# Performance work log

Measured on AMD Instinct MI355X. Metric: run time of the kernel, lower is better.

Reference implementation:

```python
import jax, jax.numpy as jnp
import numpy as np

NLAYERS, NHEADS, NFEAT, HDIM = 2, 8, 512, 64
ALPHA = 0.2
NEG = -9e15


def setup_inputs() -> dict:
    key = jax.random.key(0)
    ks = jax.random.split(key, 20)
    B, Ng, Nc, Nq = 4, 1024, 1024, 256
    s = 0.05
    inp = {
        "gloss": jax.random.normal(ks[0], (B, Ng, NFEAT), jnp.float32),
        "clip": jax.random.normal(ks[1], (B, Nc, NFEAT), jnp.float32),
        "question": jax.random.normal(ks[2], (B, Nq, NFEAT), jnp.float32),
        "gloss2clipadj": jax.random.randint(ks[3], (B, Ng, Nc), 0, 2, jnp.int32),
        "gloss2questionadj": jax.random.randint(ks[4], (B, Ng, Nq), 0, 2, jnp.int32),
    }
    # per-layer, per-head attention params: W [L,H,F,D], a split halves a1/a2 [L,H,D]
    for i, name in enumerate(["c2g", "g2q", "q2g"]):
        inp[name + "_W"] = jax.random.normal(ks[5 + i], (NLAYERS, NHEADS, NFEAT, HDIM), jnp.float32) * s
        inp[name + "_a1"] = jax.random.normal(ks[8 + i], (NLAYERS, NHEADS, HDIM), jnp.float32) * s
        inp[name + "_a2"] = jax.random.normal(ks[11 + i], (NLAYERS, NHEADS, HDIM), jnp.float32) * s
    # 4 FusionLayers per encoder layer (G2C, C2G, G2Q, Q2G), each with W,U,Wf,Uf [F,F]
    for i, name in enumerate(["fus_W", "fus_U", "fus_Wf", "fus_Uf"]):
        inp[name] = jax.random.normal(ks[14 + i], (NLAYERS, 4, NFEAT, NFEAT), jnp.float32) * s
    return inp


def _attn(q, kv, adj, W, a1, a2):
    # multi-head GAT-style additive cross attention; W [H,F,D], q [B,N,F], kv [B,M,F], adj [B,N,M]
    Wq = jnp.einsum('bnf,hfd->bhnd', q, W)
    Wk = jnp.einsum('bmf,hfd->bhmd', kv, W)
    e = jax.nn.leaky_relu(
        jnp.einsum('bhnd,hd->bhn', Wq, a1)[:, :, :, None]
        + jnp.einsum('bhmd,hd->bhm', Wk, a2)[:, :, None, :], ALPHA)
    e = jnp.where(adj[:, None, :, :] > 0, e, NEG)
    att = jax.nn.softmax(e, axis=2)  # torch F.softmax(dim=1) on [B,N,M]: query axis (faithful)
    h = jax.nn.elu(jnp.einsum('bhnm,bhmd->bhnd', att, Wk))
    B, H, N, D = h.shape
    return jnp.transpose(h, (0, 2, 1, 3)).reshape(B, N, H * D)  # concat heads


def _fusion(a, b, W, U, Wf, Uf):
    new_a = a @ W + b @ U
    f = jax.nn.sigmoid(a @ Wf + b @ Uf)
    return f * new_a + (1.0 - f) * a  # dropout is identity at inference


def reference(gloss, clip, question, gloss2clipadj, gloss2questionadj,
              c2g_W, c2g_a1, c2g_a2, g2q_W, g2q_a1, g2q_a2, q2g_W, q2g_a1, q2g_a2,
              fus_W, fus_U, fus_Wf, fus_Uf):
    g2c_f = gloss2clipadj.astype(gloss.dtype)
    g2q_T = jnp.transpose(gloss2questionadj, (0, 2, 1))
    for l in range(NLAYERS):
        gloss_same = jnp.einsum('bnm,bnf->bmf', g2c_f, gloss)  # adj^T @ gloss
        clip_1 = _fusion(clip, gloss_same, fus_W[l, 0], fus_U[l, 0], fus_Wf[l, 0], fus_Uf[l, 0])
        clip_agg = _attn(gloss, clip, gloss2clipadj, c2g_W[l], c2g_a1[l], c2g_a2[l])
        gloss_1 = _fusion(gloss, clip_agg, fus_W[l, 1], fus_U[l, 1], fus_Wf[l, 1], fus_Uf[l, 1])
        gloss_agg = _attn(question, gloss, g2q_T, g2q_W[l], g2q_a1[l], g2q_a2[l])
        question_1 = _fusion(question, gloss_agg, fus_W[l, 2], fus_U[l, 2], fus_Wf[l, 2], fus_Uf[l, 2])
        question_agg = _attn(gloss, question, gloss2questionadj, q2g_W[l], q2g_a1[l], q2g_a2[l])
        gloss_2 = _fusion(gloss_1, question_agg, fus_W[l, 3], fus_U[l, 3], fus_Wf[l, 3], fus_Uf[l, 3])
        gloss, clip, question = gloss_2, clip_1, question_1
    return gloss, clip, question
```

## Files before the change

### kernel.cpp

```cpp
#include <hip/hip_runtime.h>
#include <math.h>

#define NFEAT 512
#define NHEADS 8
#define HDIM 64
#define NB 4
#define NG 1024
#define NC 1024
#define NQ 256
#define NEGV -9e15f
#define CHUNKS 16
#define FF ((size_t)NFEAT*NFEAT)
#define LSTR 36
#define SEG 2304

typedef _Float16 v8h __attribute__((ext_vector_type(8)));
typedef float v4f __attribute__((ext_vector_type(4)));
#define MFMA16(a,b,c) __builtin_amdgcn_mfma_f32_16x16x32_f16((a),(b),(c),0,0,0)

#define GLDS(g, l) __builtin_amdgcn_global_load_lds( \
    (__attribute__((address_space(1))) void*)(g), \
    (__attribute__((address_space(3))) void*)(l), 16, 0, 0)

__device__ __forceinline__ int ldsw(int row, int quad){
    return row*32 + (((quad) ^ ((row>>1)&3)) << 3);
}

__device__ __forceinline__ float lrelu(float x){ return fmaxf(x, 0.2f*x); }
__device__ __forceinline__ unsigned short f2h(float x){ union{_Float16 h; unsigned short u;} v; v.h = (_Float16)x; return v.u; }
__device__ __forceinline__ float h2f(unsigned short u){ union{_Float16 h; unsigned short u;} v; v.u = u; return (float)v.h; }

__global__ __launch_bounds__(256) void cvt_h_k(const float* __restrict__ src, unsigned short* __restrict__ dst){
    int idx = blockIdx.x*256 + threadIdx.x;
    const float4* s = (const float4*)(src + (size_t)idx*8);
    float4 a = s[0], b = s[1];
    ushort4 p0{f2h(a.x),f2h(a.y),f2h(a.z),f2h(a.w)};
    ushort4 p1{f2h(b.x),f2h(b.y),f2h(b.z),f2h(b.w)};
    *(ushort4*)(dst + (size_t)idx*8) = p0;
    *(ushort4*)(dst + (size_t)idx*8 + 4) = p1;
}

__global__ __launch_bounds__(256) void cvt_hl_k(const float* __restrict__ src,
    unsigned short* __restrict__ dstHi, unsigned short* __restrict__ dstLo){
    int idx = blockIdx.x*256 + threadIdx.x;
// ... 64 lines not shown
        int idx = (r & 15)*256 + tid;
        int h = idx >> 9;
        const float* Wp = W + (size_t)idx*64;
        float s1 = 0.f, s2 = 0.f;
        #pragma unroll
        for (int d = 0; d < 64; ++d){ float w = Wp[d]; s1 += w*a1[(h<<6)+d]; s2 += w*a2[(h<<6)+d]; }
        wa13[a*4096 + idx] = s1; wa23[a*4096 + idx] = s2;
        return;
    }
    int a = bx >> 6, bxl = bx & 63;
    const float* W = (a==0?W0:a==1?W1:W2);
    unsigned short* WT = WT3 + (size_t)a*FF;
    int h = bxl >> 3, f0 = (bxl & 7)*64;
    __shared__ float sT[64][65];
    #pragma unroll
    for (int it = 0; it < 4; ++it){
        int idx = it*256 + tid;
        int r = idx >> 4, c4 = idx & 15;
        float4 v = *(const float4*)(W + ((size_t)h*512 + f0 + r)*64 + c4*4);
        sT[r][c4*4+0]=v.x; sT[r][c4*4+1]=v.y; sT[r][c4*4+2]=v.z; sT[r][c4*4+3]=v.w;
    }
    __syncthreads();
    #pragma unroll
    for (int it = 0; it < 2; ++it){
        int idx = it*256 + tid;
        int dd = idx >> 3, c8 = idx & 7;
        ushort4 p0{f2h(sT[c8*8+0][dd]),f2h(sT[c8*8+1][dd]),f2h(sT[c8*8+2][dd]),f2h(sT[c8*8+3][dd])};
        ushort4 p1{f2h(sT[c8*8+4][dd]),f2h(sT[c8*8+5][dd]),f2h(sT[c8*8+6][dd]),f2h(sT[c8*8+7][dd])};
        unsigned short* o = WT + ((size_t)h*64 + dd)*512 + f0 + c8*8;
        *(ushort4*)o = p0; *(ushort4*)(o+4) = p1;
    }
}

__global__ __launch_bounds__(256) void adjT_h_k(const int* __restrict__ adj, unsigned short* __restrict__ dst){
    int b = blockIdx.z;
    int c0 = blockIdx.x*64, g0 = blockIdx.y*64;
    __shared__ int sI[64][65];
    int tid = threadIdx.x;
    #pragma unroll
    for (int it = 0; it < 4; ++it){
        int idx = it*256 + tid;
        int r = idx >> 4, c4 = idx & 15;
        int4 v = *(const int4*)(adj + ((size_t)b*NG + g0 + r)*NC + c0 + c4*4);
        sI[r][c4*4+0]=v.x; sI[r][c4*4+1]=v.y; sI[r][c4*4+2]=v.z; sI[r][c4*4+3]=v.w;
    }
    __syncthreads();
    #pragma unroll
    for (int it = 0; it < 2; ++it){
        int idx = it*256 + tid;
        int dd = idx >> 3, c8 = idx & 7;
        ushort4 p0, p1;
        #pragma unroll
        for (int j = 0; j < 4; ++j) (&p0.x)[j] = sI[c8*8+j][dd] > 0 ? (unsigned short)0x3C00 : (unsigned short)0;
        #pragma unroll
        for (int j = 0; j < 4; ++j) (&p1.x)[j] = sI[c8*8+4+j][dd] > 0 ? (unsigned short)0x3C00 : (unsigned short)0;
        unsigned short* o = dst + ((size_t)b*NC + c0 + dd)*NG + g0 + c8*8;
        *(ushort4*)o = p0; *(ushort4*)(o+4) = p1;
    }
}

__global__ __launch_bounds__(256) void adjT_int_k(const int* __restrict__ adj, int* __restrict__ dst){
    int b = blockIdx.z;
    int q0 = blockIdx.x*64, g0 = blockIdx.y*64;
    __shared__ int sI[64][65];
    int tid = threadIdx.x;
    #pragma unroll
    for (int it = 0; it < 4; ++it){
        int idx = it*256 + tid;
        int r = idx >> 4, c4 = idx & 15;
        int4 v = *(const int4*)(adj + ((size_t)b*NG + g0 + r)*NQ + q0 + c4*4);
        sI[r][c4*4+0]=v.x; sI[r][c4*4+1]=v.y; sI[r][c4*4+2]=v.z; sI[r][c4*4+3]=v.w;
    }
    __syncthreads();
    #pragma unroll
    for (int it = 0; it < 4; ++it){
        int idx = it*256 + tid;
        int dd = idx >> 4, c4 = idx & 15;
        int4 v{sI[c4*4+0][dd], sI[c4*4+1][dd], sI[c4*4+2][dd], sI[c4*4+3][dd]};
        *(int4*)(dst + ((size_t)b*NQ + q0 + dd)*NG + g0 + c4*4) = v;
    }
}

__global__ __launch_bounds__(256) void bm_int_k(const int* __restrict__ adj, unsigned long long* __restrict__ out){
    int w = threadIdx.x >> 6, lane = threadIdx.x & 63;
    #pragma unroll
    for (int i = 0; i < 4; ++i){
        size_t seg = (size_t)blockIdx.x*16 + i*4 + w;
        int v = adj[seg*64 + lane];
        unsigned long long m = __ballot(v > 0);
        if (lane == 0) out[seg] = m;
    }
}

__global__ __launch_bounds__(256) void bm_h_k(const unsigned short* __restrict__ adj, unsigned long long* __restrict__ out){
    int w = threadIdx.x >> 6, lane = threadIdx.x & 63;
    #pragma unroll
    for (int i = 0; i < 4; ++i){
        size_t seg = (size_t)blockIdx.x*16 + i*4 + w;
        unsigned short v = adj[seg*64 + lane];
        unsigned long long m = __ballot(v != 0);
        if (lane == 0) out[seg] = m;
    }
}

__global__ __launch_bounds__(256) void actT_hl_k(const float* __restrict__ src,
    unsigned short* __restrict__ dstHi, unsigned short* __restrict__ dstLo, int Nrows){
    int b = blockIdx.z;
    int f0 = blockIdx.x*64, g0 = blockIdx.y*64;
    __shared__ float sF[64][65];
    int tid = threadIdx.x;
    #pragma unroll
    for (int it = 0; it < 4; ++it){
        int idx = it*256 + tid;
        int r = idx >> 4, c4 = idx & 15;
        float4 v = *(const float4*)(src + ((size_t)b*Nrows + g0 + r)*512 + f0 + c4*4);
        sF[r][c4*4+0]=v.x; sF[r][c4*4+1]=v.y; sF[r][c4*4+2]=v.z; sF[r][c4*4+3]=v.w;
    }
    __syncthreads();
    #pragma unroll
    for (int it = 0; it < 2; ++it){
        int idx = it*256 + tid;
        int dd = idx >> 3, c8 = idx & 7;
        unsigned short hi[8], lo[8];
        #pragma unroll
        for (int j = 0; j < 8; ++j){
            float x = sF[c8*8+j][dd];
            hi[j] = f2h(x);
            lo[j] = f2h(x - h2f(hi[j]));
        }
        size_t oo = ((size_t)b*512 + f0 + dd)*Nrows + g0 + c8*8;
        *(ushort4*)(dstHi+oo)   = ushort4{hi[0],hi[1],hi[2],hi[3]};
        *(ushort4*)(dstHi+oo+4) = ushort4{hi[4],hi[5],hi[6],hi[7]};
        *(ushort4*)(dstLo+oo)   = ushort4{lo[0],lo[1],lo[2],lo[3]};
        *(ushort4*)(dstLo+oo+4) = ushort4{lo[4],lo[5],lo[6],lo[7]};
    }
}

__global__ __launch_bounds__(256) void scores3_k(
    const unsigned short* __restrict__ g, const unsigned short* __restrict__ c,
    const unsigned short* __restrict__ q,
    const float* __restrict__ wa13, const float* __restrict__ wa23,
    float* __restrict__ qs3, float* __restrict__ ks3){
    int lane = threadIdx.x & 63;
    int grow = blockIdx.x*4 + (threadIdx.x >> 6);
    int b = grow / 4608; int r = grow - b*4608;
    const unsigned short* X; const float* wa; float* out; int n, oOff, rowsX;
    if (r < SEG){
        out = qs3;
        if (r < 1024)      { X=g; wa=wa13;        n=r;        oOff=0;    rowsX=NG; }
        else if (r < 1280) { X=q; wa=wa13+4096;   n=r-1024;   oOff=1024; rowsX=NQ; }
        else               { X=g; wa=wa13+8192;   n=r-1280;   oOff=1280; rowsX=NG; }
    } else {
        out = ks3; r -= SEG;
        if (r < 1024)      { X=c; wa=wa23;        n=r;        oOff=0;    rowsX=NC; }
        else if (r < 2048) { X=g; wa=wa23+4096;   n=r-1024;   oOff=1024; rowsX=NG; }
        else               { X=q; wa=wa23+8192;   n=r-2048;   oOff=2048; rowsX=NQ; }
    }
    const unsigned short* Xr = X + ((size_t)b*rowsX + n)*NFEAT;
    float p[NHEADS];
    #pragma unroll
    for (int h = 0; h < NHEADS; ++h) p[h] = 0.f;
    #pragma unroll
    for (int cc = 0; cc < 8; ++cc){
        float x = h2f(Xr[(cc<<6) + lane]);
        #pragma unroll
        for (int h = 0; h < NHEADS; ++h) p[h] += x * wa[(h<<9) + (cc<<6) + lane];
    }
// ... 28 lines not shown
    size_t aRow = (size_t)(r0 + sr)*512 + sq*8;
    size_t bRow = (size_t)(c0 + sr)*512 + sq*8;
    v4f acc[4];
    #pragma unroll
    for (int cf = 0; cf < 4; ++cf) acc[cf] = (v4f)0.f;
    GLDS(aG + aRow, &aS[0][w << 9]);
    GLDS(bG + bRow, &bS[0][w << 9]);
    __syncthreads();
    int buf = 0;
    for (int s = 0; s < 16; ++s){
        if (s < 15){
            int ktn = (s + 1) << 5;
            GLDS(aG + aRow + ktn, &aS[buf^1][w << 9]);
            GLDS(bG + bRow + ktn, &bS[buf^1][w << 9]);
        }
        v8h af = *(const v8h*)&aS[buf][ldsw(w*16 + lrow, quad)];
        #pragma unroll
        for (int cf = 0; cf < 4; ++cf){
            v8h bf = *(const v8h*)&bS[buf][ldsw(cf*16 + lrow, quad)];
            acc[cf] = MFMA16(af, bf, acc[cf]);
        }
        __syncthreads();
        buf ^= 1;
    }
    #pragma unroll
    for (int cf = 0; cf < 4; ++cf){
        int colg = c0 + cf*16 + lrow;
        int rbase = r0 + w*16 + quad*4;
        ushort4 pk{f2h(acc[cf][0]), f2h(acc[cf][1]), f2h(acc[cf][2]), f2h(acc[cf][3])};
        *(ushort4*)&WkT3[((size_t)b*512 + colg)*SEG + mOff + rbase] = pk;
    }
}

__global__ __launch_bounds__(256) void colstat3_k(
    const unsigned* __restrict__ bm_cg, const unsigned* __restrict__ bm_gq,
    const unsigned* __restrict__ bm_qg,
    const float* __restrict__ qs3, const float* __restrict__ ks3,
    float* __restrict__ pcm, float* __restrict__ psum){
    int x = blockIdx.x, b = blockIdx.z;
    const unsigned* bm; int Mrows, N, N32, mOff, qOff;
    if (x < 256)      { bm=bm_cg; Mrows=NC; N=NG; N32=NG/32; mOff=0;    qOff=0; }
    else if (x < 512) { x-=256; bm=bm_gq; Mrows=NG; N=NQ; N32=NQ/32; mOff=1024; qOff=1024; }
    else              { x-=512; bm=bm_qg; Mrows=NQ; N=NG; N32=NG/32; mOff=2048; qOff=1280; }
    int mt = x >> 4, ch = x & 15;
    int chunk = N / CHUNKS, subl = chunk >> 2;
    int ml = threadIdx.x & 63; int m = mt*64 + ml;
    int g = threadIdx.x >> 6;
    int n0 = ch*chunk + g*subl;
    __shared__ float sQ[64][8];
    for (int t2 = threadIdx.x; t2 < chunk*8; t2 += 256)
        sQ[t2>>3][t2&7] = qs3[((size_t)b*SEG + qOff + ch*chunk)*8 + t2];
    float ksv[8];
    size_t mo = ((size_t)b*SEG + mOff + m)*8;
    #pragma unroll
    for (int h = 0; h < 8; ++h) ksv[h] = ks3[mo+h];
    unsigned word = bm[((size_t)b*Mrows + m)*N32 + (n0>>5)];
    unsigned bits = (word >> (n0 & 31)) & ((1u << subl) - 1u);
    __syncthreads();
    int nb = g*subl;
    float mx[8];
    #pragma unroll
    for (int h = 0; h < 8; ++h) mx[h] = -INFINITY;
    for (int i = 0; i < subl; ++i){
        if ((bits >> i) & 1){
            #pragma unroll
            for (int h = 0; h < 8; ++h) mx[h] = fmaxf(mx[h], sQ[nb+i][h]);
        }
    }
    float cm[8], s[8];
    #pragma unroll
    for (int h = 0; h < 8; ++h){
        cm[h] = bits ? lrelu(mx[h] + ksv[h]) : NEGV;
        s[h] = 0.f;
    }
    for (int i = 0; i < subl; ++i){
        bool on = (bits >> i) & 1;
        #pragma unroll
        for (int h = 0; h < 8; ++h){
            float e = on ? lrelu(sQ[nb+i][h] + ksv[h]) : NEGV;
            s[h] += __expf(e - cm[h]);
        }
    }
    __shared__ float scm[4][64][8], ssm[4][64][8];
    #pragma unroll
    for (int h = 0; h < 8; ++h){ scm[g][ml][h] = cm[h]; ssm[g][ml][h] = s[h]; }
    __syncthreads();
    if (g == 0){
        #pragma unroll
        for (int h = 0; h < 8; ++h){
            float c0 = scm[0][ml][h], c1 = scm[1][ml][h], c2 = scm[2][ml][h], c3 = scm[3][ml][h];
            float CM = fmaxf(fmaxf(c0, c1), fmaxf(c2, c3));
            float S = ssm[0][ml][h]*__expf(c0-CM) + ssm[1][ml][h]*__expf(c1-CM)
                    + ssm[2][ml][h]*__expf(c2-CM) + ssm[3][ml][h]*__expf(c3-CM);
            size_t o = (((size_t)b*CHUNKS + ch)*SEG + mOff + m)*8 + h;
            pcm[o] = CM; psum[o] = S;
        }
    }
}

__global__ __launch_bounds__(256) void colfin3_k(const float* __restrict__ pcm, const float* __restrict__ psum,
    const float* __restrict__ ks3, float* __restrict__ ksh, float* __restrict__ cmh,
    float* __restrict__ ish){
    int idx = blockIdx.x*256 + threadIdx.x;
    const int m8 = SEG*8;
    int b = idx / m8, rem = idx - b*m8;
    int m = rem >> 3, h = rem & 7;
    size_t base = (size_t)b*CHUNKS*m8 + rem;
    float c[CHUNKS], s[CHUNKS];
    #pragma unroll
    for (int ch = 0; ch < CHUNKS; ++ch){
        c[ch] = pcm[base + (size_t)ch*m8];
        s[ch] = psum[base + (size_t)ch*m8];
    }
    float CM = c[0];
    #pragma unroll
    for (int ch = 1; ch < CHUNKS; ++ch) CM = fmaxf(CM, c[ch]);
    float S = 0.f;
    #pragma unroll
    for (int ch = 0; ch < CHUNKS; ++ch) S += s[ch]*__expf(c[ch] - CM);
    size_t o = ((size_t)b*8 + h)*SEG + m;
    ksh[o] = ks3[idx]; cmh[o] = CM; ish[o] = 1.f/S;
}

template<int MULTI>
__global__ __launch_bounds__(256) void fusion_all_k(
    const unsigned short* __restrict__ aHi, const unsigned short* __restrict__ aLo,
    const unsigned short* __restrict__ bHi, const unsigned short* __restrict__ bLo,
    const unsigned short* __restrict__ Whi, const unsigned short* __restrict__ Wlo,
    unsigned short* __restrict__ dst, unsigned short* __restrict__ dstLo,
    unsigned short* __restrict__ dstT, unsigned short* __restrict__ dstTLo,
    float* __restrict__ dstF, int rows){
    int nY = rows >> 6;
    int ppg = (nY * NB) >> 3;
    int F = blockIdx.x;
    int xcd = F & 7, t = F >> 3;
    int c0i = t / ppg;
    int p = xcd + ((t - c0i*ppg) << 3);
    int r0 = (p % nY) << 6, c0 = c0i << 6;
    int b = p / nY;
    int tid = threadIdx.x;
    __shared__ alignas(16) unsigned short aHs[2048], bHs[2048];
    __shared__ alignas(16) unsigned short aLs[MULTI ? 2048 : 16], bLs[MULTI ? 2048 : 16];
    __shared__ alignas(16) unsigned short wHs[8192];
    __shared__ alignas(16) unsigned short wLs[MULTI ? 8192 : 16];
    size_t actOff = (size_t)b*rows*512;
    const unsigned short* aHG = aHi + actOff;
    const unsigned short* bHG = bHi + actOff;
    const unsigned short* aLG = aLo ? aLo + actOff : nullptr;
    const unsigned short* bLG = bLo ? bLo + actOff : nullptr;
    bool hasALo = MULTI && (aLG != nullptr);
    bool hasBLo = MULTI && (bLG != nullptr);
    int w = tid >> 6, lane = tid & 63;
    int wr = w >> 1, wc = w & 1;
    int lrow = lane & 15, quad = lane >> 4;
    int sr = tid >> 2;
    int sq = (tid & 3) ^ ((sr >> 1) & 3);
    size_t aRow = (size_t)(r0 + sr)*512 + sq*8;
    size_t wPk = (size_t)c0i*16*8192 + (size_t)sr*32 + sq*8;
    unsigned short* ldsA  = &aHs[w << 9];
    unsigned short* ldsB  = &bHs[w << 9];
    unsigned short* ldsAL = &aLs[MULTI ? (w << 9) : 0];
    unsigned short* ldsBL = &bLs[MULTI ? (w << 9) : 0];
    v4f accN[2][2], accF[2][2];
    #pragma unroll
    for (int r = 0; r < 2; ++r)
        #pragma unroll
        for (int cf = 0; cf < 2; ++cf){ accN[r][cf] = (v4f)0.f; accF[r][cf] = (v4f)0.f; }
    for (int kt = 0; kt < 512; kt += 32){
        __syncthreads();
        GLDS(aHG + aRow + kt, ldsA);
        GLDS(bHG + aRow + kt, ldsB);
        if (hasALo) GLDS(aLG + aRow + kt, ldsAL);
        if (hasBLo) GLDS(bLG + aRow + kt, ldsBL);
        size_t wk = wPk + (size_t)(kt >> 5)*8192;
        #pragma unroll
        for (int m = 0; m < 4; ++m){
            GLDS(Whi + wk + (m<<11), &wHs[(m<<11) + (w<<9)]);
            if (MULTI) GLDS(Wlo + wk + (m<<11), &wLs[MULTI ? ((m<<11) + (w<<9)) : 0]);
        }
        __syncthreads();
        v8h ah[2], bh[2], al[2], bl[2];
        #pragma unroll
        for (int r = 0; r < 2; ++r){
            int ao = ldsw(wr*32 + r*16 + lrow, quad);
            ah[r] = *(const v8h*)&aHs[ao];
            bh[r] = *(const v8h*)&bHs[ao];
            if (hasALo) al[r] = *(const v8h*)&aLs[ao];
            if (hasBLo) bl[r] = *(const v8h*)&bLs[ao];
        }
        #pragma unroll
        for (int cf = 0; cf < 2; ++cf){
            int wo = ldsw(wc*32 + cf*16 + lrow, quad);
            v8h w0 = *(const v8h*)&wHs[wo];
            v8h w1 = *(const v8h*)&wHs[2048 + wo];
            v8h w2 = *(const v8h*)&wHs[4096 + wo];
            v8h w3 = *(const v8h*)&wHs[6144 + wo];
            v8h l0, l1, l2, l3;
            if (MULTI){
                l0 = *(const v8h*)&wLs[wo];
                l1 = *(const v8h*)&wLs[2048 + wo];
                l2 = *(const v8h*)&wLs[4096 + wo];
                l3 = *(const v8h*)&wLs[6144 + wo];
            }
            #pragma unroll
            for (int r = 0; r < 2; ++r){
                accN[r][cf] = MFMA16(ah[r], w0, accN[r][cf]);
                accN[r][cf] = MFMA16(bh[r], w1, accN[r][cf]);
                accF[r][cf] = MFMA16(ah[r], w2, accF[r][cf]);
                accF[r][cf] = MFMA16(bh[r], w3, accF[r][cf]);
                if (MULTI){
                    if (hasALo){ accN[r][cf] = MFMA16(al[r], w0, accN[r][cf]); accF[r][cf] = MFMA16(al[r], w2, accF[r][cf]); }
                    if (hasBLo){ accN[r][cf] = MFMA16(bl[r], w1, accN[r][cf]); accF[r][cf] = MFMA16(bl[r], w3, accF[r][cf]); }
                    accN[r][cf] = MFMA16(ah[r], l0, accN[r][cf]);
                    accN[r][cf] = MFMA16(bh[r], l1, accN[r][cf]);
                    accF[r][cf] = MFMA16(ah[r], l2, accF[r][cf]);
                    accF[r][cf] = MFMA16(bh[r], l3, accF[r][cf]);
                }
            }
        }
    }
    #pragma unroll
    for (int r = 0; r < 2; ++r)
        #pragma unroll
        for (int cf = 0; cf < 2; ++cf){
            int colg = c0 + wc*32 + cf*16 + lrow;
            int rbase = r0 + wr*32 + r*16 + quad*4;
            float o4[4];
            #pragma unroll
            for (int reg = 0; reg < 4; ++reg){
                float f = 1.f/(1.f + __expf(-accF[r][cf][reg]));
                size_t ai = (size_t)(rbase+reg)*512 + colg;
                float ao = h2f(aHG[ai]);
                if (aLG) ao += h2f(aLG[ai]);
                o4[reg] = f*accN[r][cf][reg] + (1.f - f)*ao;
                size_t oo = ((size_t)b*rows + rbase + reg)*512 + colg;
                unsigned short hv = f2h(o4[reg]);
                dst[oo] = hv;
                if (dstLo) dstLo[oo] = f2h(o4[reg] - h2f(hv));
                if (dstF) dstF[oo] = o4[reg];
            }
            if (dstT){
                unsigned short h0 = f2h(o4[0]), h1 = f2h(o4[1]), h2 = f2h(o4[2]), h3 = f2h(o4[3]);
                size_t to = ((size_t)b*512 + colg)*rows + rbase;
                *(ushort4*)&dstT[to] = ushort4{h0,h1,h2,h3};
                if (dstTLo)
                    *(ushort4*)&dstTLo[to] = ushort4{f2h(o4[0]-h2f(h0)), f2h(o4[1]-h2f(h1)),
                                                     f2h(o4[2]-h2f(h2)), f2h(o4[3]-h2f(h3))};
            }
        }
}

__global__ __launch_bounds__(256) void gemmT_mfma_k(
    const unsigned short* __restrict__ A, size_t aStride,
    const unsigned short* __restrict__ BT, const unsigned short* __restrict__ BT2, size_t bStride,
    int K, int rowsPB,
    unsigned short* __restrict__ outRM, unsigned short* __restrict__ outLo,
    unsigned short* __restrict__ outT){
    int b = blockIdx.z;
    int r0 = blockIdx.y*64, c0 = blockIdx.x*64;
    int tid = threadIdx.x;
    __shared__ alignas(16) unsigned short aS[2][2048], bS[2][2048];
    const unsigned short* aG = A + (size_t)b*aStride;
    const unsigned short* bG0 = BT + (size_t)b*bStride;
    const unsigned short* bG1 = BT2 ? BT2 + (size_t)b*bStride : nullptr;
    int w = tid >> 6, lane = tid & 63;
    int lrow = lane & 15, quad = lane >> 4;
    int sr = tid >> 2;
    int sq = (tid & 3) ^ ((sr >> 1) & 3);
    size_t aRow = (size_t)(r0 + sr)*K + sq*8;
    size_t bRow = (size_t)(c0 + sr)*K + sq*8;
    int spp = K >> 5;
    int nsteps = (BT2 ? 2 : 1)*spp;
    v4f acc[4];
    #pragma unroll
    for (int cf = 0; cf < 4; ++cf) acc[cf] = (v4f)0.f;
    GLDS(aG + aRow, &aS[0][w << 9]);
    GLDS(bG0 + bRow, &bS[0][w << 9]);
    __syncthreads();
    int buf = 0;
    for (int s = 0; s < nsteps; ++s){
// ... 162 lines not shown
    const float* in_gloss = (const float*)d_in[0];
    const float* in_clip  = (const float*)d_in[1];
    const float* in_q     = (const float*)d_in[2];
    const int*   adj_gc   = (const int*)d_in[3];
    const int*   adj_gq   = (const int*)d_in[4];
    const float* c2gW  = (const float*)d_in[5];
    const float* c2ga1 = (const float*)d_in[6];
    const float* c2ga2 = (const float*)d_in[7];
    const float* g2qW  = (const float*)d_in[8];
    const float* g2qa1 = (const float*)d_in[9];
    const float* g2qa2 = (const float*)d_in[10];
    const float* q2gW  = (const float*)d_in[11];
    const float* q2ga1 = (const float*)d_in[12];
    const float* q2ga2 = (const float*)d_in[13];
    const float* fusW  = (const float*)d_in[14];
    const float* fusU  = (const float*)d_in[15];
    const float* fusWf = (const float*)d_in[16];
    const float* fusUf = (const float*)d_in[17];
    float* out = (float*)d_out;
    float* out_gloss = out;
    float* out_clip  = out + (size_t)NB*NG*NFEAT;
    float* out_q     = out + (size_t)NB*NG*NFEAT*2;

    char* wsB = (char*)d_ws;
    size_t off = 0;
    auto alloc = [&](size_t bytes){ void* p = wsB + off; off += (bytes + 255) & ~(size_t)255; return p; };
    float* wa13  = (float*)alloc(3*4096*4);
    float* wa23  = (float*)alloc(3*4096*4);
    float* qs3   = (float*)alloc((size_t)NB*SEG*8*4);
    float* ks3   = (float*)alloc((size_t)NB*SEG*8*4);
    float* ksh3  = (float*)alloc((size_t)NB*8*SEG*4);
    float* cmh3  = (float*)alloc((size_t)NB*8*SEG*4);
    float* ish3  = (float*)alloc((size_t)NB*8*SEG*4);
    float* pcm   = (float*)alloc((size_t)NB*CHUNKS*SEG*8*4);
    float* psum  = (float*)alloc((size_t)NB*CHUNKS*SEG*8*4);
    unsigned short* WflatT3 = (unsigned short*)alloc((size_t)3*FF*2);
    unsigned short* WkT3    = (unsigned short*)alloc((size_t)NB*512*SEG*2);
    unsigned short* wtAll   = (unsigned short*)alloc((size_t)32*FF*2);
    unsigned short* wtAllLo = (unsigned short*)alloc((size_t)32*FF*2);
    unsigned short* adjTgc  = (unsigned short*)alloc((size_t)NB*NC*NG*2);
    unsigned short* g_bf0   = (unsigned short*)alloc((size_t)NB*NG*NFEAT*2);
    unsigned short* gLo0    = (unsigned short*)alloc((size_t)NB*NG*NFEAT*2);
    unsigned short* g_bf1   = (unsigned short*)alloc((size_t)NB*NG*NFEAT*2);
    unsigned short* gLo1    = (unsigned short*)alloc((size_t)NB*NG*NFEAT*2);
    unsigned short* gT      = (unsigned short*)alloc((size_t)NB*NFEAT*NG*2);
    unsigned short* gTlo    = (unsigned short*)alloc((size_t)NB*NFEAT*NG*2);
    unsigned short* gA_bf   = (unsigned short*)alloc((size_t)NB*NG*NFEAT*2);
    unsigned short* gALo    = (unsigned short*)alloc((size_t)NB*NG*NFEAT*2);
    unsigned short* c_bf0   = (unsigned short*)alloc((size_t)NB*NC*NFEAT*2);
    unsigned short* cLo0    = (unsigned short*)alloc((size_t)NB*NC*NFEAT*2);
    unsigned short* c_bf1   = (unsigned short*)alloc((size_t)NB*NC*NFEAT*2);
    unsigned short* cLo1    = (unsigned short*)alloc((size_t)NB*NC*NFEAT*2);
    unsigned short* q_bf0   = (unsigned short*)alloc((size_t)NB*NQ*NFEAT*2);
    unsigned short* q_bf1   = (unsigned short*)alloc((size_t)NB*NQ*NFEAT*2);
    unsigned short* agg_bf  = (unsigned short*)alloc((size_t)NB*NG*NFEAT*2);
    unsigned short* aggLo   = (unsigned short*)alloc((size_t)NB*NG*NFEAT*2);
    int* adjTgq = (int*)alloc((size_t)NB*NQ*NG*4);
    unsigned* bm_gc = (unsigned*)alloc((size_t)NB*NG*(NC/32)*4);
    unsigned* bm_cg = (unsigned*)alloc((size_t)NB*NC*(NG/32)*4);
    unsigned* bm_gq = (unsigned*)alloc((size_t)NB*NG*(NQ/32)*4);
    unsigned* bm_qg = (unsigned*)alloc((size_t)NB*NQ*(NG/32)*4);
    (void)ws_size; (void)in_sizes; (void)n_in; (void)out_size;

    const size_t HFD = (size_t)NHEADS*NFEAT*HDIM;
    const size_t HD  = (size_t)NHEADS*HDIM;

    wtT_k<<<2048, 256, 0, stream>>>(fusW, fusU, fusWf, fusUf, wtAll, wtAllLo);
    adjT_h_k<<<dim3(NC/64, NG/64, NB), 256, 0, stream>>>(adj_gc, adjTgc);
    adjT_int_k<<<dim3(NQ/64, NG/64, NB), 256, 0, stream>>>(adj_gq, adjTgq);
    bm_int_k<<<(NB*NG*NC/64)/16, 256, 0, stream>>>(adj_gc, (unsigned long long*)bm_gc);
    bm_int_k<<<(NB*NG*NQ/64)/16, 256, 0, stream>>>(adj_gq, (unsigned long long*)bm_gq);
    bm_int_k<<<(NB*NQ*NG/64)/16, 256, 0, stream>>>(adjTgq, (unsigned long long*)bm_qg);
    bm_h_k<<<(NB*NC*NG/64)/16, 256, 0, stream>>>(adjTgc, (unsigned long long*)bm_cg);
    cvt_hl_k<<<(NB*NG*NFEAT)/2048, 256, 0, stream>>>(in_gloss, g_bf0, gLo0);
    cvt_hl_k<<<(NB*NC*NFEAT)/2048, 256, 0, stream>>>(in_clip,  c_bf0, cLo0);
    cvt_h_k<<<(NB*NQ*NFEAT)/2048, 256, 0, stream>>>(in_q,     q_bf0);
    actT_hl_k<<<dim3(8, NG/64, NB), 256, 0, stream>>>(in_gloss, gT, gTlo, NG);

    auto run_fusion = [&](const unsigned short* a, const unsigned short* aLo,
                          const unsigned short* bb, const unsigned short* bLo, int rows,
                          int l, int i, int npass,
                          unsigned short* dst, unsigned short* dstLo,
                          unsigned short* dstT, unsigned short* dstTLo, float* dstF){
        const unsigned short* Whi = wtAll   + (size_t)((l*4 + i)*4)*FF;
        const unsigned short* Wlo = wtAllLo + (size_t)((l*4 + i)*4)*FF;
        if (npass == 3)
            fusion_all_k<1><<<dim3(8*(rows/64)*NB), 256, 0, stream>>>(
                a, aLo, bb, bLo, Whi, Wlo, dst, dstLo, dstT, dstTLo, dstF, rows);
        else
            fusion_all_k<0><<<dim3(8*(rows/64)*NB), 256, 0, stream>>>(
                a, aLo, bb, bLo, Whi, Wlo, dst, dstLo, dstT, dstTLo, dstF, rows);
    };

    for (int l = 0; l < 2; ++l){
        const unsigned short* g_cur = (l == 0) ? g_bf0 : g_bf1;
        const unsigned short* gLoC  = (l == 0) ? gLo0  : gLo1;
        const unsigned short* c_cur = (l == 0) ? c_bf0 : c_bf1;
        const unsigned short* cLoC  = (l == 0) ? cLo0  : cLo1;
        const unsigned short* q_cur = (l == 0) ? q_bf0 : q_bf1;
        unsigned short* g_nxt = (l == 0) ? g_bf1 : g_bf0;
        unsigned short* gLoN  = (l == 0) ? gLo1  : nullptr;
        unsigned short* c_nxt = (l == 0) ? c_bf1 : c_bf0;
        unsigned short* cLoN  = (l == 0) ? cLo1  : nullptr;
        unsigned short* q_nxt = (l == 0) ? q_bf1 : q_bf0;
        float* gF = (l == 1) ? out_gloss : nullptr;
        float* cF = (l == 1) ? out_clip  : nullptr;
        float* qF = (l == 1) ? out_q     : nullptr;

        prep_attnW3_k<<<240, 256, 0, stream>>>(
            c2gW + l*HFD, c2ga1 + l*HD, c2ga2 + l*HD,
            g2qW + l*HFD, g2qa1 + l*HD, g2qa2 + l*HD,
            q2gW + l*HFD, q2ga1 + l*HD, q2ga2 + l*HD,
            WflatT3, wa13, wa23);
        scores3_k<<<(NB*4608)/4, 256, 0, stream>>>(g_cur, c_cur, q_cur, wa13, wa23, qs3, ks3);
        wkt3_mfma_k<<<dim3(8, 36, NB), 256, 0, stream>>>(c_cur, g_cur, q_cur, WflatT3, WkT3);
        colstat3_k<<<dim3(576, 1, NB), 256, 0, stream>>>(bm_cg, bm_gq, bm_qg, qs3, ks3, pcm, psum);
        colfin3_k<<<(NB*SEG*8)/256, 256, 0, stream>>>(pcm, psum, ks3, ksh3, cmh3, ish3);

        gemmT_mfma_k<<<dim3(8, NC/64, NB), 256, 0, stream>>>(adjTgc, (size_t)NC*NG, gT, gTlo,
                                                             (size_t)512*NG, NG, NC,
                                                             agg_bf, aggLo, nullptr);
        run_fusion(c_cur, cLoC, agg_bf, aggLo, NC, l, 0, 3,
                   c_nxt, cLoN, nullptr, nullptr, cF);
        attn_mfma_k<<<(NG/64)*32, 256, 0, stream>>>(bm_gc, NC/32, qs3, 0, ksh3, cmh3, ish3, 0,
                                                    WkT3, agg_bf, NG, NC);
        run_fusion(g_cur, gLoC, agg_bf, nullptr, NG, l, 1, 1,
                   gA_bf, gALo, nullptr, nullptr, nullptr);
        attn_mfma_k<<<(NQ/64)*32, 256, 0, stream>>>(bm_qg, NG/32, qs3, 1024, ksh3, cmh3, ish3, 1024,
                                                    WkT3, agg_bf, NQ, NG);
        run_fusion(q_cur, nullptr, agg_bf, nullptr, NQ, l, 2, 1,
                   q_nxt, nullptr, nullptr, nullptr, qF);
        attn_mfma_k<<<(NG/64)*32, 256, 0, stream>>>(bm_gq, NQ/32, qs3, 1280, ksh3, cmh3, ish3, 2048,
                                                    WkT3, agg_bf, NG, NQ);
        run_fusion(gA_bf, gALo, agg_bf, nullptr, NG, l, 3, 3,
                   g_nxt, gLoN, (l == 0) ? gT : nullptr, (l == 0) ? gTlo : nullptr, gF);
    }
}
```

Measured before the change: 699.3 us.

## Fuse bitmask builds into transposes, merge column stats, add pipelined single-pass fusion kernel

The separate bitmask kernels are removed; the adjacency transpose kernels now also emit row and column bitmasks from their shared tiles. The gloss fp16 hi/lo conversion is folded into the transpose kernel. The two-stage column softmax statistics (chunked partials plus a finalize kernel) become a single kernel that computes the global max first and then the exp-sums. A new double-buffered single-pass fusion GEMM kernel replaces the templated variant for the npass==1 cases. This trades fewer launches and less intermediate traffic for much less parallelism in the column-stat kernel (144 blocks instead of 2304), each doing serial loops over up to 1024 entries.

Measured after the change: 906.0 us. 29.6% more time.

```diff
diff --git a/kernel.cpp b/kernel.cpp
--- a/kernel.cpp
+++ b/kernel.cpp
@@ -9,7 +9,6 @@
 #define NC 1024
 #define NQ 256
 #define NEGV -9e15f
-#define CHUNKS 16
 #define FF ((size_t)NFEAT*NFEAT)
 #define LSTR 36
 #define SEG 2304
@@ -140,7 +139,8 @@
     }
 }
 
-__global__ __launch_bounds__(256) void adjT_h_k(const int* __restrict__ adj, unsigned short* __restrict__ dst){
+__global__ __launch_bounds__(256) void adjT_h_k(const int* __restrict__ adj, unsigned short* __restrict__ dst,
+    unsigned long long* __restrict__ bm_gc, unsigned long long* __restrict__ bm_cg){
     int b = blockIdx.z;
     int c0 = blockIdx.x*64, g0 = blockIdx.y*64;
     __shared__ int sI[64][65];
@@ -153,6 +153,7 @@
         sI[r][c4*4+0]=v.x; sI[r][c4*4+1]=v.y; sI[r][c4*4+2]=v.z; sI[r][c4*4+3]=v.w;
     }
     __syncthreads();
+    int wv = tid >> 6, lane = tid & 63;
     #pragma unroll
     for (int it = 0; it < 2; ++it){
         int idx = it*256 + tid;
@@ -165,9 +166,20 @@
         unsigned short* o = dst + ((size_t)b*NC + c0 + dd)*NG + g0 + c8*8;
         *(ushort4*)o = p0; *(ushort4*)(o+4) = p1;
     }
-}
-
-__global__ __launch_bounds__(256) void adjT_int_k(const int* __restrict__ adj, int* __restrict__ dst){
+    #pragma unroll
+    for (int rr = wv; rr < 64; rr += 4){
+        unsigned long long m = __ballot(sI[rr][lane] > 0);
+        if (lane == 0) bm_gc[((size_t)b*NG + g0 + rr)*(NC/64) + (c0>>6)] = m;
+    }
+    #pragma unroll
+    for (int cc = wv; cc < 64; cc += 4){
+        unsigned long long m = __ballot(sI[lane][cc] > 0);
+        if (lane == 0) bm_cg[((size_t)b*NC + c0 + cc)*(NG/64) + (g0>>6)] = m;
+    }
+}
+
+__global__ __launch_bounds__(256) void adjT_int_k(const int* __restrict__ adj, int* __restrict__ dst,
+    unsigned long long* __restrict__ bm_gq, unsigned long long* __restrict__ bm_qg){
     int b = blockIdx.z;
     int q0 = blockIdx.x*64, g0 = blockIdx.y*64;
     __shared__ int sI[64][65];
@@ -180,6 +192,7 @@
         sI[r][c4*4+0]=v.x; sI[r][c4*4+1]=v.y; sI[r][c4*4+2]=v.z; sI[r][c4*4+3]=v.w;
     }
     __syncthreads();
+    int wv = tid >> 6, lane = tid & 63;
     #pragma unroll
     for (int it = 0; it < 4; ++it){
         int idx = it*256 + tid;
@@ -187,32 +200,21 @@
         int4 v{sI[c4*4+0][dd], sI[c4*4+1][dd], sI[c4*4+2][dd], sI[c4*4+3][dd]};
         *(int4*)(dst + ((size_t)b*NQ + q0 + dd)*NG + g0 + c4*4) = v;
     }
-}
-
-__global__ __launch_bounds__(256) void bm_int_k(const int* __restrict__ adj, unsigned long long* __restrict__ out){
-    int w = threadIdx.x >> 6, lane = threadIdx.x & 63;
-    #pragma unroll
-    for (int i = 0; i < 4; ++i){
-        size_t seg = (size_t)blockIdx.x*16 + i*4 + w;
-        int v = adj[seg*64 + lane];
-        unsigned long long m = __ballot(v > 0);
-        if (lane == 0) out[seg] = m;
-    }
-}
-
-__global__ __launch_bounds__(256) void bm_h_k(const unsigned short* __restrict__ adj, unsigned long long* __restrict__ out){
-    int w = threadIdx.x >> 6, lane = threadIdx.x & 63;
-    #pragma unroll
-    for (int i = 0; i < 4; ++i){
-        size_t seg = (size_t)blockIdx.x*16 + i*4 + w;
-        unsigned short v = adj[seg*64 + lane];
-        unsigned long long m = __ballot(v != 0);
-        if (lane == 0) out[seg] = m;
+    #pragma unroll
+    for (int rr = wv; rr < 64; rr += 4){
+        unsigned long long m = __ballot(sI[rr][lane] > 0);
+        if (lane == 0) bm_gq[((size_t)b*NG + g0 + rr)*(NQ/64) + (q0>>6)] = m;
+    }
+    #pragma unroll
+    for (int cc = wv; cc < 64; cc += 4){
+        unsigned long long m = __ballot(sI[lane][cc] > 0);
+        if (lane == 0) bm_qg[((size_t)b*NQ + q0 + cc)*(NG/64) + (g0>>6)] = m;
     }
 }
 
 __global__ __launch_bounds__(256) void actT_hl_k(const float* __restrict__ src,
-    unsigned short* __restrict__ dstHi, unsigned short* __restrict__ dstLo, int Nrows){
+    unsigned short* __restrict__ dstHi, unsigned short* __restrict__ dstLo,
+    unsigned short* __restrict__ rmHi, unsigned short* __restrict__ rmLo, int Nrows){
     int b = blockIdx.z;
     int f0 = blockIdx.x*64, g0 = blockIdx.y*64;
     __shared__ float sF[64][65];
@@ -241,6 +243,23 @@
         *(ushort4*)(dstHi+oo+4) = ushort4{hi[4],hi[5],hi[6],hi[7]};
         *(ushort4*)(dstLo+oo)   = ushort4{lo[0],lo[1],lo[2],lo[3]};
         *(ushort4*)(dstLo+oo+4) = ushort4{lo[4],lo[5],lo[6],lo[7]};
+    }
+    #pragma unroll
+    for (int it = 0; it < 2; ++it){
+        int idx = it*256 + tid;
+        int r = idx >> 3, c8 = idx & 7;
+        unsigned short hi[8], lo[8];
+        #pragma unroll
+        for (int j = 0; j < 8; ++j){
+            float x = sF[r][c8*8+j];
+            hi[j] = f2h(x);
+            lo[j] = f2h(x - h2f(hi[j]));
+        }
+        size_t oo = ((size_t)b*Nrows + g0 + r)*512 + f0 + c8*8;
+        *(ushort4*)(rmHi+oo)   = ushort4{hi[0],hi[1],hi[2],hi[3]};
+        *(ushort4*)(rmHi+oo+4) = ushort4{hi[4],hi[5],hi[6],hi[7]};
+        *(ushort4*)(rmLo+oo)   = ushort4{lo[0],lo[1],lo[2],lo[3]};
+        *(ushort4*)(rmLo+oo+4) = ushort4{lo[4],lo[5],lo[6],lo[7]};
     }
 }
 
@@ -335,98 +354,96 @@
     }
 }
 
-__global__ __launch_bounds__(256) void colstat3_k(
+__global__ __launch_bounds__(256) void colstat3b_k(
     const unsigned* __restrict__ bm_cg, const unsigned* __restrict__ bm_gq,
     const unsigned* __restrict__ bm_qg,
     const float* __restrict__ qs3, const float* __restrict__ ks3,
-    float* __restrict__ pcm, float* __restrict__ psum){
+    float* __restrict__ ksh, float* __restrict__ cmh, float* __restrict__ ish){
     int x = blockIdx.x, b = blockIdx.z;
     const unsigned* bm; int Mrows, N, N32, mOff, qOff;
-    if (x < 256)      { bm=bm_cg; Mrows=NC; N=NG; N32=NG/32; mOff=0;    qOff=0; }
-    else if (x < 512) { x-=256; bm=bm_gq; Mrows=NG; N=NQ; N32=NQ/32; mOff=1024; qOff=1024; }
-    else              { x-=512; bm=bm_qg; Mrows=NQ; N=NG; N32=NG/32; mOff=2048; qOff=1280; }
-    int mt = x >> 4, ch = x & 15;
-    int chunk = N / CHUNKS, subl = chunk >> 2;
-    int ml = threadIdx.x & 63; int m = mt*64 + ml;
+    if (x < 16)      { bm=bm_cg; Mrows=NC; N=NG; N32=NG/32; mOff=0;    qOff=0; }
+    else if (x < 32) { x-=16; bm=bm_gq; Mrows=NG; N=NQ; N32=NQ/32; mOff=1024; qOff=1024; }
+    else             { x-=32; bm=bm_qg; Mrows=NQ; N=NG; N32=NG/32; mOff=2048; qOff=1280; }
+    int ml = threadIdx.x & 63; int m = x*64 + ml;
     int g = threadIdx.x >> 6;
-    int n0 = ch*chunk + g*subl;
-    __shared__ float sQ[64][8];
-    for (int t2 = threadIdx.x; t2 < chunk*8; t2 += 256)
-        sQ[t2>>3][t2&7] = qs3[((size_t)b*SEG + qOff + ch*chunk)*8 + t2];
+    int len = N >> 2;
+    int n0 = g*len;
+    __shared__ float sQ[1024*8];
+    {
+        const float* qb = qs3 + ((size_t)b*SEG + qOff)*8;
+        for (int t4 = threadIdx.x; t4 < N*2; t4 += 256)
+            *(float4*)&sQ[t4*4] = *(const float4*)(qb + t4*4);
+    }
     float ksv[8];
     size_t mo = ((size_t)b*SEG + mOff + m)*8;
     #pragma unroll
     for (int h = 0; h < 8; ++h) ksv[h] = ks3[mo+h];
-    unsigned word = bm[((size_t)b*Mrows + m)*N32 + (n0>>5)];
-    unsigned bits = (word >> (n0 & 31)) & ((1u << subl) - 1u);
-    __syncthreads();
-    int nb = g*subl;
+    const unsigned* bmr = bm + ((size_t)b*Mrows + m)*N32 + (n0>>5);
+    int nw = len >> 5;
     float mx[8];
     #pragma unroll
     for (int h = 0; h < 8; ++h) mx[h] = -INFINITY;
-    for (int i = 0; i < subl; ++i){
-        if ((bits >> i) & 1){
-            #pragma unroll
-            for (int h = 0; h < 8; ++h) mx[h] = fmaxf(mx[h], sQ[nb+i][h]);
-        }
-    }
-    float cm[8], s[8];
-    #pragma unroll
-    for (int h = 0; h < 8; ++h){
-        cm[h] = bits ? lrelu(mx[h] + ksv[h]) : NEGV;
-        s[h] = 0.f;
-    }
-    for (int i = 0; i < subl; ++i){
-        bool on = (bits >> i) & 1;
+    unsigned anyw = 0;
+    __syncthreads();
+    for (int wI = 0; wI < nw; ++wI){
+        unsigned wd = bmr[wI];
+        anyw |= wd;
+        if (!wd) continue;
+        int base = n0 + wI*32;
+        for (int i2 = 0; i2 < 32; ++i2){
+            if ((wd >> i2) & 1){
+                const float* qr = &sQ[(base+i2)*8];
+                #pragma unroll
+                for (int h = 0; h < 8; ++h) mx[h] = fmaxf(mx[h], qr[h]);
+            }
+        }
+    }
+    __shared__ float scm[4][64][8], ssm[4][64][8];
+    #pragma unroll
+    for (int h = 0; h < 8; ++h) scm[g][ml][h] = anyw ? mx[h] : -INFINITY;
+    __syncthreads();
+    __shared__ float sCM[64][8];
+    if (g == 0){
         #pragma unroll
         for (int h = 0; h < 8; ++h){
-            float e = on ? lrelu(sQ[nb+i][h] + ksv[h]) : NEGV;
-            s[h] += __expf(e - cm[h]);
-        }
-    }
-    __shared__ float scm[4][64][8], ssm[4][64][8];
-    #pragma unroll
-    for (int h = 0; h < 8; ++h){ scm[g][ml][h] = cm[h]; ssm[g][ml][h] = s[h]; }
+            float am = fmaxf(fmaxf(scm[0][ml][h], scm[1][ml][h]), fmaxf(scm[2][ml][h], scm[3][ml][h]));
+            sCM[ml][h] = (am == -INFINITY) ? NEGV : lrelu(am + ksv[h]);
+        }
+    }
+    __syncthreads();
+    float CM[8];
+    #pragma unroll
+    for (int h = 0; h < 8; ++h) CM[h] = sCM[ml][h];
+    float s[8];
+    #pragma unroll
+    for (int h = 0; h < 8; ++h) s[h] = 0.f;
+    for (int wI = 0; wI < nw; ++wI){
+        unsigned wd = bmr[wI];
+        int base = n0 + wI*32;
+        for (int i2 = 0; i2 < 32; ++i2){
+            bool on = (wd >> i2) & 1;
+            const float* qr = &sQ[(base+i2)*8];
+            #pragma unroll
+            for (int h = 0; h < 8; ++h){
+                float e = on ? lrelu(qr[h] + ksv[h]) : NEGV;
+                s[h] += __expf(e - CM[h]);
+            }
+        }
+    }
+    #pragma unroll
+    for (int h = 0; h < 8; ++h) ssm[g][ml][h] = s[h];
     __syncthreads();
     if (g == 0){
         #pragma unroll
         for (int h = 0; h < 8; ++h){
-            float c0 = scm[0][ml][h], c1 = scm[1][ml][h], c2 = scm[2][ml][h], c3 = scm[3][ml][h];
-            float CM = fmaxf(fmaxf(c0, c1), fmaxf(c2, c3));
-            float S = ssm[0][ml][h]*__expf(c0-CM) + ssm[1][ml][h]*__expf(c1-CM)
-                    + ssm[2][ml][h]*__expf(c2-CM) + ssm[3][ml][h]*__expf(c3-CM);
-            size_t o = (((size_t)b*CHUNKS + ch)*SEG + mOff + m)*8 + h;
-            pcm[o] = CM; psum[o] = S;
-        }
-    }
-}
-
-__global__ __launch_bounds__(256) void colfin3_k(const float* __restrict__ pcm, const float* __restrict__ psum,
-    const float* __restrict__ ks3, float* __restrict__ ksh, float* __restrict__ cmh,
-    float* __restrict__ ish){
-    int idx = blockIdx.x*256 + threadIdx.x;
-    const int m8 = SEG*8;
-    int b = idx / m8, rem = idx - b*m8;
-    int m = rem >> 3, h = rem & 7;
-    size_t base = (size_t)b*CHUNKS*m8 + rem;
-    float c[CHUNKS], s[CHUNKS];
-    #pragma unroll
-    for (int ch = 0; ch < CHUNKS; ++ch){
-        c[ch] = pcm[base + (size_t)ch*m8];
-        s[ch] = psum[base + (size_t)ch*m8];
-    }
-    float CM = c[0];
-    #pragma unroll
-    for (int ch = 1; ch < CHUNKS; ++ch) CM = fmaxf(CM, c[ch]);
-    float S = 0.f;
-    #pragma unroll
-    for (int ch = 0; ch < CHUNKS; ++ch) S += s[ch]*__expf(c[ch] - CM);
-    size_t o = ((size_t)b*8 + h)*SEG + m;
-    ksh[o] = ks3[idx]; cmh[o] = CM; ish[o] = 1.f/S;
-}
-
-template<int MULTI>
-__global__ __launch_bounds__(256) void fusion_all_k(
+            float S = ssm[0][ml][h] + ssm[1][ml][h] + ssm[2][ml][h] + ssm[3][ml][h];
+            size_t o = ((size_t)b*8 + h)*SEG + mOff + m;
+            ksh[o] = ksv[h]; cmh[o] = CM[h]; ish[o] = 1.f/S;
+        }
+    }
+}
+
+__global__ __launch_bounds__(256) void fusion3_k(
     const unsigned short* __restrict__ aHi, const unsigned short* __restrict__ aLo,
     const unsigned short* __restrict__ bHi, const unsigned short* __restrict__ bLo,
     const unsigned short* __restrict__ Whi, const unsigned short* __restrict__ Wlo,
@@ -442,17 +459,15 @@
     int r0 = (p % nY) << 6, c0 = c0i << 6;
     int b = p / nY;
     int tid = threadIdx.x;
-    __shared__ alignas(16) unsigned short aHs[2048], bHs[2048];
-    __shared__ alignas(16) unsigned short aLs[MULTI ? 2048 : 16], bLs[MULTI ? 2048 : 16];
-    __shared__ alignas(16) unsigned short wHs[8192];
-    __shared__ alignas(16) unsigned short wLs[MULTI ? 8192 : 16];
+    __shared__ alignas(16) unsigned short aHs[2048], bHs[2048], aLs[2048], bLs[2048];
+    __shared__ alignas(16) unsigned short wHs[8192], wLs[8192];
     size_t actOff = (size_t)b*rows*512;
     const unsigned short* aHG = aHi + actOff;
     const unsigned short* bHG = bHi + actOff;
     const unsigned short* aLG = aLo ? aLo + actOff : nullptr;
     const unsigned short* bLG = bLo ? bLo + actOff : nullptr;
-    bool hasALo = MULTI && (aLG != nullptr);
-    bool hasBLo = MULTI && (bLG != nullptr);
+    bool hasALo = (aLG != nullptr);
+    bool hasBLo = (bLG != nullptr);
     int w = tid >> 6, lane = tid & 63;
     int wr = w >> 1, wc = w & 1;
     int lrow = lane & 15, quad = lane >> 4;
@@ -462,8 +477,8 @@
     size_t wPk = (size_t)c0i*16*8192 + (size_t)sr*32 + sq*8;
     unsigned short* ldsA  = &aHs[w << 9];
     unsigned short* ldsB  = &bHs[w << 9];
-    unsigned short* ldsAL = &aLs[MULTI ? (w << 9) : 0];
-    unsigned short* ldsBL = &bLs[MULTI ? (w << 9) : 0];
+    unsigned short* ldsAL = &aLs[w << 9];
+    unsigned short* ldsBL = &bLs[w << 9];
     v4f accN[2][2], accF[2][2];
     #pragma unroll
     for (int r = 0; r < 2; ++r)
@@ -479,7 +494,7 @@
         #pragma unroll
         for (int m = 0; m < 4; ++m){
             GLDS(Whi + wk + (m<<11), &wHs[(m<<11) + (w<<9)]);
-            if (MULTI) GLDS(Wlo + wk + (m<<11), &wLs[MULTI ? ((m<<11) + (w<<9)) : 0]);
+            GLDS(Wlo + wk + (m<<11), &wLs[(m<<11) + (w<<9)]);
         }
         __syncthreads();
         v8h ah[2], bh[2], al[2], bl[2];
@@ -498,27 +513,22 @@
             v8h w1 = *(const v8h*)&wHs[2048 + wo];
             v8h w2 = *(const v8h*)&wHs[4096 + wo];
             v8h w3 = *(const v8h*)&wHs[6144 + wo];
-            v8h l0, l1, l2, l3;
-            if (MULTI){
-                l0 = *(const v8h*)&wLs[wo];
-                l1 = *(const v8h*)&wLs[2048 + wo];
-                l2 = *(const v8h*)&wLs[4096 + wo];
-                l3 = *(const v8h*)&wLs[6144 + wo];
-            }
+            v8h l0 = *(const v8h*)&wLs[wo];
+            v8h l1 = *(const v8h*)&wLs[2048 + wo];
+            v8h l2 = *(const v8h*)&wLs[4096 + wo];
+            v8h l3 = *(const v8h*)&wLs[6144 + wo];
             #pragma unroll
             for (int r = 0; r < 2; ++r){
                 accN[r][cf] = MFMA16(ah[r], w0, accN[r][cf]);
                 accN[r][cf] = MFMA16(bh[r], w1, accN[r][cf]);
                 accF[r][cf] = MFMA16(ah[r], w2, accF[r][cf]);
                 accF[r][cf] = MFMA16(bh[r], w3, accF[r][cf]);
-                if (MULTI){
-                    if (hasALo){ accN[r][cf] = MFMA16(al[r], w0, accN[r][cf]); accF[r][cf] = MFMA16(al[r], w2, accF[r][cf]); }
-                    if (hasBLo){ accN[r][cf] = MFMA16(bl[r], w1, accN[r][cf]); accF[r][cf] = MFMA16(bl[r], w3, accF[r][cf]); }
-                    accN[r][cf] = MFMA16(ah[r], l0, accN[r][cf]);
-                    accN[r][cf] = MFMA16(bh[r], l1, accN[r][cf]);
-                    accF[r][cf] = MFMA16(ah[r], l2, accF[r][cf]);
-                    accF[r][cf] = MFMA16(bh[r], l3, accF[r][cf]);
-                }
+                if (hasALo){ accN[r][cf] = MFMA16(al[r], w0, accN[r][cf]); accF[r][cf] = MFMA16(al[r], w2, accF[r][cf]); }
+                if (hasBLo){ accN[r][cf] = MFMA16(bl[r], w1, accN[r][cf]); accF[r][cf] = MFMA16(bl[r], w3, accF[r][cf]); }
+                accN[r][cf] = MFMA16(ah[r], l0, accN[r][cf]);
+                accN[r][cf] = MFMA16(bh[r], l1, accN[r][cf]);
+                accF[r][cf] = MFMA16(ah[r], l2, accF[r][cf]);
+                accF[r][cf] = MFMA16(bh[r], l3, accF[r][cf]);
             }
         }
     }
@@ -549,6 +559,103 @@
                 if (dstTLo)
                     *(ushort4*)&dstTLo[to] = ushort4{f2h(o4[0]-h2f(h0)), f2h(o4[1]-h2f(h1)),
                                                      f2h(o4[2]-h2f(h2)), f2h(o4[3]-h2f(h3))};
+            }
+        }
+}
+
+__global__ __launch_bounds__(256) void fusion1_k(
+    const unsigned short* __restrict__ aHi, const unsigned short* __restrict__ aLo,
+    const unsigned short* __restrict__ bHi,
+    const unsigned short* __restrict__ Whi,
+    unsigned short* __restrict__ dst, unsigned short* __restrict__ dstLo,
+    float* __restrict__ dstF, int rows){
+    int nY = rows >> 6;
+    int ppg = (nY * NB) >> 3;
+    int F = blockIdx.x;
+    int xcd = F & 7, t = F >> 3;
+    int c0i = t / ppg;
+    int p = xcd + ((t - c0i*ppg) << 3);
+    int r0 = (p % nY) << 6, c0 = c0i << 6;
+    int b = p / nY;
+    int tid = threadIdx.x;
+    __shared__ alignas(16) unsigned short aHs[2][2048], bHs[2][2048];
+    __shared__ alignas(16) unsigned short wHs[2][8192];
+    size_t actOff = (size_t)b*rows*512;
+    const unsigned short* aHG = aHi + actOff;
+    const unsigned short* bHG = bHi + actOff;
+    const unsigned short* aLG = aLo ? aLo + actOff : nullptr;
+    int w = tid >> 6, lane = tid & 63;
+    int wr = w >> 1, wc = w & 1;
+    int lrow = lane & 15, quad = lane >> 4;
+    int sr = tid >> 2;
+    int sq = (tid & 3) ^ ((sr >> 1) & 3);
+    size_t aRow = (size_t)(r0 + sr)*512 + sq*8;
+    size_t wPk = (size_t)c0i*16*8192 + (size_t)sr*32 + sq*8;
+    v4f accN[2][2], accF[2][2];
+    #pragma unroll
+    for (int r = 0; r < 2; ++r)
+        #pragma unroll
+        for (int cf = 0; cf < 2; ++cf){ accN[r][cf] = (v4f)0.f; accF[r][cf] = (v4f)0.f; }
+
+    #define F1STAGE(bb, kk) do{ \
+        GLDS(aHG + aRow + (kk), &aHs[bb][w << 9]); \
+        GLDS(bHG + aRow + (kk), &bHs[bb][w << 9]); \
+        size_t wk_ = wPk + (size_t)((kk) >> 5)*8192; \
+        GLDS(Whi + wk_,          &wHs[bb][(0<<11) + (w<<9)]); \
+        GLDS(Whi + wk_ + (1<<11), &wHs[bb][(1<<11) + (w<<9)]); \
+        GLDS(Whi + wk_ + (2<<11), &wHs[bb][(2<<11) + (w<<9)]); \
+        GLDS(Whi + wk_ + (3<<11), &wHs[bb][(3<<11) + (w<<9)]); \
+    } while(0)
+
+    F1STAGE(0, 0);
+    __syncthreads();
+    int buf = 0;
+    for (int kt = 0; kt < 512; kt += 32){
+        if (kt + 32 < 512) F1STAGE(buf^1, kt + 32);
+        v8h ah[2], bh[2];
+        #pragma unroll
+        for (int r = 0; r < 2; ++r){
+            int ao = ldsw(wr*32 + r*16 + lrow, quad);
+            ah[r] = *(const v8h*)&aHs[buf][ao];
+            bh[r] = *(const v8h*)&bHs[buf][ao];
+        }
+        #pragma unroll
+        for (int cf = 0; cf < 2; ++cf){
+            int wo = ldsw(wc*32 + cf*16 + lrow, quad);
+            v8h w0 = *(const v8h*)&wHs[buf][wo];
+            v8h w1 = *(const v8h*)&wHs[buf][2048 + wo];
+            v8h w2 = *(const v8h*)&wHs[buf][4096 + wo];
+            v8h w3 = *(const v8h*)&wHs[buf][6144 + wo];
+            #pragma unroll
+            for (int r = 0; r < 2; ++r){
+                accN[r][cf] = MFMA16(ah[r], w0, accN[r][cf]);
+                accN[r][cf] = MFMA16(bh[r], w1, accN[r][cf]);
+                accF[r][cf] = MFMA16(ah[r], w2, accF[r][cf]);
+                accF[r][cf] = MFMA16(bh[r], w3, accF[r][cf]);
+            }
+        }
+        __syncthreads();
+        buf ^= 1;
+    }
+    #undef F1STAGE
+    #pragma unroll
+    for (int r = 0; r < 2; ++r)
+        #pragma unroll
+        for (int cf = 0; cf < 2; ++cf){
+            int colg = c0 + wc*32 + cf*16 + lrow;
+            int rbase = r0 + wr*32 + r*16 + quad*4;
+            #pragma unroll
+            for (int reg = 0; reg < 4; ++reg){
+                float f = 1.f/(1.f + __expf(-accF[r][cf][reg]));
+                size_t ai = (size_t)(rbase+reg)*512 + colg;
+                float ao = h2f(aHG[ai]);
+                if (aLG) ao += h2f(aLG[ai]);
+                float o = f*accN[r][cf][reg] + (1.f - f)*ao;
+                size_t oo = ((size_t)b*rows + rbase + reg)*512 + colg;
+                unsigned short hv = f2h(o);
+                dst[oo] = hv;
+                if (dstLo) dstLo[oo] = f2h(o - h2f(hv));
+                if (dstF) dstF[oo] = o;
             }
         }
 }
@@ -777,8 +884,6 @@
     float* ksh3  = (float*)alloc((size_t)NB*8*SEG*4);
     float* cmh3  = (float*)alloc((size_t)NB*8*SEG*4);
     float* ish3  = (float*)alloc((size_t)NB*8*SEG*4);
-    float* pcm   = (float*)alloc((size_t)NB*CHUNKS*SEG*8*4);
-    float* psum  = (float*)alloc((size_t)NB*CHUNKS*SEG*8*4);
     unsigned short* WflatT3 = (unsigned short*)alloc((size_t)3*FF*2);
     unsigned short* WkT3    = (unsigned short*)alloc((size_t)NB*512*SEG*2);
     unsigned short* wtAll   = (unsigned short*)alloc((size_t)32*FF*2);
@@ -811,16 +916,13 @@
     const size_t HD  = (size_t)NHEADS*HDIM;
 
     wtT_k<<<2048, 256, 0, stream>>>(fusW, fusU, fusWf, fusUf, wtAll, wtAllLo);
-    adjT_h_k<<<dim3(NC/64, NG/64, NB), 256, 0, stream>>>(adj_gc, adjTgc);
-    adjT_int_k<<<dim3(NQ/64, NG/64, NB), 256, 0, stream>>>(adj_gq, adjTgq);
-    bm_int_k<<<(NB*NG*NC/64)/16, 256, 0, stream>>>(adj_gc, (unsigned long long*)bm_gc);
-    bm_int_k<<<(NB*NG*NQ/64)/16, 256, 0, stream>>>(adj_gq, (unsigned long long*)bm_gq);
-    bm_int_k<<<(NB*NQ*NG/64)/16, 256, 0, stream>>>(adjTgq, (unsigned long long*)bm_qg);
-    bm_h_k<<<(NB*NC*NG/64)/16, 256, 0, stream>>>(adjTgc, (unsigned long long*)bm_cg);
-    cvt_hl_k<<<(NB*NG*NFEAT)/2048, 256, 0, stream>>>(in_gloss, g_bf0, gLo0);
+    adjT_h_k<<<dim3(NC/64, NG/64, NB), 256, 0, stream>>>(adj_gc, adjTgc,
+        (unsigned long long*)bm_gc, (unsigned long long*)bm_cg);
+    adjT_int_k<<<dim3(NQ/64, NG/64, NB), 256, 0, stream>>>(adj_gq, adjTgq,
+        (unsigned long long*)bm_gq, (unsigned long long*)bm_qg);
     cvt_hl_k<<<(NB*NC*NFEAT)/2048, 256, 0, stream>>>(in_clip,  c_bf0, cLo0);
     cvt_h_k<<<(NB*NQ*NFEAT)/2048, 256, 0, stream>>>(in_q,     q_bf0);
-    actT_hl_k<<<dim3(8, NG/64, NB), 256, 0, stream>>>(in_gloss, gT, gTlo, NG);
+    actT_hl_k<<<dim3(8, NG/64, NB), 256, 0, stream>>>(in_gloss, gT, gTlo, g_bf0, gLo0, NG);
 
     auto run_fusion = [&](const unsigned short* a, const unsigned short* aLo,
                           const unsigned short* bb, const unsigned short* bLo, int rows,
@@ -830,11 +932,11 @@
         const unsigned short* Whi = wtAll   + (size_t)((l*4 + i)*4)*FF;
         const unsigned short* Wlo = wtAllLo + (size_t)((l*4 + i)*4)*FF;
         if (npass == 3)
-            fusion_all_k<1><<<dim3(8*(rows/64)*NB), 256, 0, stream>>>(
+            fusion3_k<<<dim3(8*(rows/64)*NB), 256, 0, stream>>>(
                 a, aLo, bb, bLo, Whi, Wlo, dst, dstLo, dstT, dstTLo, dstF, rows);
         else
-            fusion_all_k<0><<<dim3(8*(rows/64)*NB), 256, 0, stream>>>(
-                a, aLo, bb, bLo, Whi, Wlo, dst, dstLo, dstT, dstTLo, dstF, rows);
+            fusion1_k<<<dim3(8*(rows/64)*NB), 256, 0, stream>>>(
+                a, aLo, bb, Whi, dst, dstLo, dstF, rows);
     };
 
     for (int l = 0; l < 2; ++l){
@@ -859,8 +961,8 @@
             WflatT3, wa13, wa23);
         scores3_k<<<(NB*4608)/4, 256, 0, stream>>>(g_cur, c_cur, q_cur, wa13, wa23, qs3, ks3);
         wkt3_mfma_k<<<dim3(8, 36, NB), 256, 0, stream>>>(c_cur, g_cur, q_cur, WflatT3, WkT3);
-        colstat3_k<<<dim3(576, 1, NB), 256, 0, stream>>>(bm_cg, bm_gq, bm_qg, qs3, ks3, pcm, psum);
-        colfin3_k<<<(NB*SEG*8)/256, 256, 0, stream>>>(pcm, psum, ks3, ksh3, cmh3, ish3);
+        colstat3b_k<<<dim3(36, 1, NB), 256, 0, stream>>>(bm_cg, bm_gq, bm_qg, qs3, ks3,
+                                                         ksh3, cmh3, ish3);
 
         gemmT_mfma_k<<<dim3(8, NC/64, NB), 256, 0, stream>>>(adjTgc, (size_t)NC*NG, gT, gTlo,
                                                              (size_t)512*NG, NG, NC,
```
